# Kernel tuning notes

Measured on AMD Instinct MI355X. Metric: run time of the kernel, lower is better.

Reference implementation:

```python
import jax, jax.numpy as jnp
import numpy as np

Q, L = 512, 4096


def setup_inputs() -> dict:
    key = jax.random.key(0)
    ks = jax.random.split(key, 12)
    def rn(k, shape, s=0.05):
        return jax.random.normal(k, shape, jnp.float32) * s
    return {
        "reactions": jax.random.normal(ks[0], (1, Q, 256), jnp.float32),
        "protein":   jax.random.normal(ks[1], (1, L, 1024), jnp.float32),
        # conv1d(1024->256, k=1) == pointwise linear
        "Wc":  rn(ks[2], (256, 1024)), "bc":  jnp.zeros((256,), jnp.float32),
        "W1":  rn(ks[3], (64, 256)),   "b1":  jnp.zeros((64,), jnp.float32),
        "W2":  rn(ks[4], (64, 256)),   "b2":  jnp.zeros((64,), jnp.float32),
        "Wa":  rn(ks[5], (64, 64)),    "ba":  jnp.zeros((64,), jnp.float32),
        "Wpa": rn(ks[6], (64, 64)),    "bpa": jnp.zeros((64,), jnp.float32),
        "Wra": rn(ks[7], (64, 64)),    "bra": jnp.zeros((64,), jnp.float32),
        "Wf1": rn(ks[8], (256, 128)),  "bf1": jnp.zeros((256,), jnp.float32),
        "Wf2": rn(ks[9], (128, 256)),  "bf2": jnp.zeros((128,), jnp.float32),
        "Wf3": rn(ks[10], (1, 128)),   "bf3": jnp.zeros((1,), jnp.float32),
    }


def reference(reactions, protein, Wc, bc, W1, b1, W2, b2, Wa, ba,
              Wpa, bpa, Wra, bra, Wf1, bf1, Wf2, bf2, Wf3, bf3):
    # protein: [1, L, 1024] -> 1x1 conv over channels == linear -> [L, 256]
    p = jax.nn.relu(protein[0] @ Wc.T + bc)
    # reactions: [1, Q, 256] -> [Q, 64]
    r = jax.nn.relu(reactions[0] @ W2.T + b2)
    # protein tokens -> [L, 64]
    k = jax.nn.relu(p @ W1.T + b1)

    ra = r @ Wra.T + bra            # [Q, 64]
    pa = k @ Wpa.T + bpa            # [L, 64]
    # broadcast outer-sum + relu + small linear: [Q, L, 64]
    A = jax.nn.relu(ra[:, None, :] + pa[None, :, :]) @ Wa.T + ba

    r_gate = jax.nn.sigmoid(jnp.mean(A, axis=1))   # [Q, 64]
    p_gate = jax.nn.sigmoid(jnp.mean(A, axis=0))   # [L, 64]

    rxnfp = r + r * r_gate                          # [Q, 64]
    prot = jnp.max(k + k * p_gate, axis=0)          # [64]  maxpool over L

    ctx = jnp.concatenate(
        [rxnfp, jnp.broadcast_to(prot, (rxnfp.shape[0], 64))], axis=1)  # [Q,128]

    # dropout layers are identity in eval mode
    h = jax.nn.leaky_relu(ctx @ Wf1.T + bf1)
    h = jax.nn.leaky_relu(h @ Wf2.T + bf2)
    out = h @ Wf3.T + bf3
    return out.reshape(-1)                          # [Q]
```

## Files before the change

### kernel.cpp

```cpp
#include <hip/hip_runtime.h>
#include <hip/hip_bf16.h>
#include <math.h>

#define TPB 256

typedef __attribute__((ext_vector_type(8))) short s16x8;
typedef __attribute__((ext_vector_type(4))) float f32x4;

#define MFMA16(a, b, c) __builtin_amdgcn_mfma_f32_16x16x32_bf16((a), (b), (c), 0, 0, 0)

constexpr unsigned OFF_P    = 0u;
constexpr unsigned OFF_K    = OFF_P    + 4096u*256u;
constexpr unsigned OFF_PA   = OFF_K    + 4096u*64u;
constexpr unsigned OFF_R    = OFF_PA   + 4096u*64u;
constexpr unsigned OFF_RA   = OFF_R    + 512u*64u;
constexpr unsigned OFF_SR   = OFF_RA   + 512u*64u;
constexpr unsigned OFF_PMAX = OFF_SR   + 512u*64u;

__device__ __forceinline__ short f2bf(float x) {
  union { float f; unsigned u; } v; v.f = x;
  unsigned r = v.u + 0x7FFFu + ((v.u >> 16) & 1u);
  return (short)(r >> 16);
}
__device__ __forceinline__ unsigned pkbf(float a, float b) {
  __hip_bfloat162 h = __float22bfloat162_rn(make_float2(a, b));
  union { __hip_bfloat162 h2; unsigned u; } v; v.h2 = h;
  return v.u;
}
union U8 { s16x8 s; unsigned u[4]; };

__global__ __launch_bounds__(TPB, 2) void k1_gemm(
    const float* __restrict__ prot, const float* __restrict__ Wc,
    const float* __restrict__ bc,   float* __restrict__ ws)
{
  int bid = blockIdx.x;
  int tid = threadIdx.x;
  if (bid >= 512) {
    int tb = bid - 512;
    unsigned base = OFF_SR + (unsigned)tb * 16384u;
#pragma unroll
    for (int it = 0; it < 16; ++it) {
      int idx = it * TPB + tid;
      *(float4*)&ws[base + (unsigned)idx * 4u] = make_float4(0.f, 0.f, 0.f, 0.f);
    }
    if (tb == 1 && tid < 16)
      *(float4*)&ws[OFF_PMAX + tid * 4] = make_float4(0.f, 0.f, 0.f, 0.f);
    return;
  }

  __shared__ __align__(16) short Asm[32 * 72];
  __shared__ __align__(16) short Bsm[64 * 72];

  int m0 = (bid >> 2) * 32;
  int n0 = (bid & 3) * 64;
  int wave = tid >> 6, lane = tid & 63;
  int wm = (wave & 1) * 16, wn = (wave >> 1) * 32;
  int lm = lane & 15, quad = lane >> 4;

  int arow = tid >> 3, aseg = (tid & 7) * 8;
  int brow = tid >> 2, bseg = (tid & 3) * 16;

  const float* Ag = prot + (size_t)(m0 + arow) * 1024 + aseg;
  const float* Bg = Wc   + (size_t)(n0 + brow) * 1024 + bseg;

  float4 a4[2], b4[4];
#pragma unroll
  for (int i = 0; i < 2; ++i) a4[i] = *(const float4*)(Ag + i * 4);
#pragma unroll
  for (int i = 0; i < 4; ++i) b4[i] = *(const float4*)(Bg + i * 4);

  f32x4 acc[2] = {};

  for (int kc = 0; kc < 16; ++kc) {
    __syncthreads();
    {
      U8 s;
      s.u[0] = pkbf(a4[0].x, a4[0].y); s.u[1] = pkbf(a4[0].z, a4[0].w);
      s.u[2] = pkbf(a4[1].x, a4[1].y); s.u[3] = pkbf(a4[1].z, a4[1].w);
      *(s16x8*)&Asm[arow * 72 + aseg] = s.s;
    }
#pragma unroll
    for (int h = 0; h < 2; ++h) {
      U8 s;
      s.u[0] = pkbf(b4[h*2].x,   b4[h*2].y);
      s.u[1] = pkbf(b4[h*2].z,   b4[h*2].w);
      s.u[2] = pkbf(b4[h*2+1].x, b4[h*2+1].y);
      s.u[3] = pkbf(b4[h*2+1].z, b4[h*2+1].w);
      *(s16x8*)&Bsm[brow * 72 + bseg + h * 8] = s.s;
    }
    if (kc < 15) {
#pragma unroll
      for (int i = 0; i < 2; ++i) a4[i] = *(const float4*)(Ag + (kc + 1) * 64 + i * 4);
#pragma unroll
      for (int i = 0; i < 4; ++i) b4[i] = *(const float4*)(Bg + (kc + 1) * 64 + i * 4);
    }
    __syncthreads();
#pragma unroll
    for (int ks = 0; ks < 2; ++ks) {
      s16x8 af = *(const s16x8*)&Asm[(wm + lm) * 72 + ks * 32 + quad * 8];
#pragma unroll
      for (int ni = 0; ni < 2; ++ni) {
        s16x8 bfv = *(const s16x8*)&Bsm[(wn + ni * 16 + lm) * 72 + ks * 32 + quad * 8];
        acc[ni] = MFMA16(af, bfv, acc[ni]);
      }
    }
  }

#pragma unroll
  for (int ni = 0; ni < 2; ++ni) {
    int col = n0 + wn + ni * 16 + lm;
    float bcv = bc[col];
#pragma unroll
    for (int r = 0; r < 4; ++r) {
      int row = m0 + wm + quad * 4 + r;
      ws[OFF_P + (unsigned)row * 256u + col] = fmaxf(acc[ni][r] + bcv, 0.f);
    }
  }
}

__global__ __launch_bounds__(TPB, 2) void k2_heads(
    const float* __restrict__ reactions,
    const float* __restrict__ W1,  const float* __restrict__ b1,
    const float* __restrict__ W2,  const float* __restrict__ b2,
    const float* __restrict__ Wpa, const float* __restrict__ bpa,
    const float* __restrict__ Wra, const float* __restrict__ bra,
    float* __restrict__ ws)
{
  __shared__ __align__(16) short Asm[32 * 264];
  __shared__ __align__(16) short Bsm[64 * 264];
  __shared__ __align__(16) short Ksm[32 * 72];
  __shared__ __align__(16) short Wsm[64 * 72];
  int bid = blockIdx.x, tid = threadIdx.x;
  bool isProt = bid < 128;
  int row0 = (isProt ? bid : (bid - 128)) * 32;
  const float* src  = isProt ? (ws + OFF_P) : reactions;
  const float* Wst1 = isProt ? W1 : W2;
  const float* bv   = isProt ? b1 : b2;
  const float* Wst2 = isProt ? Wpa : Wra;
  const float* b2nd = isProt ? bpa : bra;
  float* out1 = ws + (isProt ? OFF_K : OFF_R);
  float* out2 = ws + (isProt ? OFF_PA : OFF_RA);

  {
    int row = tid >> 3, seg = (tid & 7) * 32;
    const float* sp = src + (size_t)(row0 + row) * 256 + seg;
    float4 f[8];
#pragma unroll
    for (int i = 0; i < 8; ++i) f[i] = *(const float4*)(sp + i * 4);
#pragma unroll
    for (int i = 0; i < 4; ++i) {
      U8 s;
      s.u[0] = pkbf(f[2*i].x,   f[2*i].y);
      s.u[1] = pkbf(f[2*i].z,   f[2*i].w);
      s.u[2] = pkbf(f[2*i+1].x, f[2*i+1].y);
      s.u[3] = pkbf(f[2*i+1].z, f[2*i+1].w);
      *(s16x8*)&Asm[row * 264 + seg + i * 8] = s.s;
    }
  }
  {
    int row = tid >> 2, seg = (tid & 3) * 64;
    const float* sp = Wst1 + (size_t)row * 256 + seg;
#pragma unroll
    for (int i = 0; i < 8; ++i) {
      float4 fa = *(const float4*)(sp + i * 8);
      float4 fb = *(const float4*)(sp + i * 8 + 4);
      U8 s;
      s.u[0] = pkbf(fa.x, fa.y); s.u[1] = pkbf(fa.z, fa.w);
      s.u[2] = pkbf(fb.x, fb.y); s.u[3] = pkbf(fb.z, fb.w);
      *(s16x8*)&Bsm[row * 264 + seg + i * 8] = s.s;
    }
  }
  {
    int row = tid >> 2, seg = (tid & 3) * 16;
    const float* sp = Wst2 + (size_t)row * 64 + seg;
#pragma unroll
    for (int i = 0; i < 2; ++i) {
      float4 fa = *(const float4*)(sp + i * 8);
      float4 fb = *(const float4*)(sp + i * 8 + 4);
      U8 s;
      s.u[0] = pkbf(fa.x, fa.y); s.u[1] = pkbf(fa.z, fa.w);
      s.u[2] = pkbf(fb.x, fb.y); s.u[3] = pkbf(fb.z, fb.w);
      *(s16x8*)&Wsm[row * 72 + seg + i * 8] = s.s;
    }
  }
  __syncthreads();

  int wave = tid >> 6, lane = tid & 63;
  int lm = lane & 15, quad = lane >> 4;
  int wm = (wave >> 1) * 16, wn = (wave & 1) * 32;

  f32x4 acc[2] = {};
#pragma unroll
  for (int kc = 0; kc < 8; ++kc) {
    s16x8 a = *(const s16x8*)&Asm[(wm + lm) * 264 + kc * 32 + quad * 8];
#pragma unroll
    for (int ni = 0; ni < 2; ++ni) {
      s16x8 b = *(const s16x8*)&Bsm[(wn + ni * 16 + lm) * 264 + kc * 32 + quad * 8];
      acc[ni] = MFMA16(a, b, acc[ni]);
    }
  }
#pragma unroll
  for (int ni = 0; ni < 2; ++ni) {
    int col = wn + ni * 16 + lm;
    float bb = bv[col];
#pragma unroll
    for (int r = 0; r < 4; ++r) {
      int row = wm + quad * 4 + r;
      float kv = fmaxf(acc[ni][r] + bb, 0.f);
      out1[(size_t)(row0 + row) * 64 + col] = kv;
      Ksm[row * 72 + col] = f2bf(kv);
    }
  }
  __syncthreads();

  f32x4 acc2[2] = {};
#pragma unroll
  for (int kc = 0; kc < 2; ++kc) {
    s16x8 a = *(const s16x8*)&Ksm[(wm + lm) * 72 + kc * 32 + quad * 8];
#pragma unroll
    for (int ni = 0; ni < 2; ++ni) {
      s16x8 b = *(const s16x8*)&Wsm[(wn + ni * 16 + lm) * 72 + kc * 32 + quad * 8];
      acc2[ni] = MFMA16(a, b, acc2[ni]);
    }
  }
#pragma unroll
  for (int ni = 0; ni < 2; ++ni) {
    int col = wn + ni * 16 + lm;
    float bb = b2nd[col];
#pragma unroll
    for (int r = 0; r < 4; ++r) {
      int row = wm + quad * 4 + r;
      out2[(size_t)(row0 + row) * 64 + col] = acc2[ni][r] + bb;
    }
  }
}

__global__ __launch_bounds__(TPB) void k3_interact(
    const float* __restrict__ Wa, const float* __restrict__ ba,
    float* __restrict__ ws)
{
  __shared__ float sm[9280];
  int bid = blockIdx.x, tid = threadIdx.x;
  int c = tid & 63, g = tid >> 6;
  const float* ra = ws + OFF_RA;
  const float* pa = ws + OFF_PA;

  if (bid < 256) {
    int qt = bid >> 3, ls = bid & 7;
    int q0 = qt * 16, l0 = ls * 512;
    float u[4], acc[4];
#pragma unroll
    for (int i = 0; i < 4; ++i) {
      u[i] = ra[(q0 + g * 4 + i) * 64u + c];
      acc[i] = 0.f;
    }
    for (int chunk = 0; chunk < 8; ++chunk) {
      unsigned base = (unsigned)(l0 + chunk * 64) * 64u;
      for (int it = 0; it < 4; ++it) {
        int i4 = it * TPB + tid;
        int row = i4 >> 4, c4 = (i4 & 15) * 4;
        *(float4*)&sm[row * 64 + c4] = *(const float4*)(pa + base + row * 64 + c4);
      }
      __syncthreads();
#pragma unroll 4
      for (int ll = 0; ll < 64; ++ll) {
        float x = sm[ll * 64 + c];
#pragma unroll
        for (int i = 0; i < 4; ++i) acc[i] += fmaxf(u[i] + x, 0.f);
      }
      __syncthreads();
    }
#pragma unroll
    for (int i = 0; i < 4; ++i)
      atomicAdd(&ws[OFF_SR + (unsigned)(q0 + g * 4 + i) * 64u + c], acc[i]);
  } else {
    int b = bid - 256;
    int l0 = b * 16;
    for (int it = 0; it < 16; ++it) {
      int idx = it * TPB + tid;
      int a = idx >> 6, bb = idx & 63;
      sm[5120 + bb * 65 + a] = Wa[idx];
    }
    float v[4], acc[4];
#pragma unroll
    for (int i = 0; i < 4; ++i) {
      v[i] = pa[(unsigned)(l0 + g * 4 + i) * 64u + c];
      acc[i] = 0.f;
    }
    for (int chunk = 0; chunk < 8; ++chunk) {
      unsigned base = (unsigned)(chunk * 64) * 64u;
      for (int it = 0; it < 4; ++it) {
        int i4 = it * TPB + tid;
        int row = i4 >> 4, c4 = (i4 & 15) * 4;
        *(float4*)&sm[row * 64 + c4] = *(const float4*)(ra + base + row * 64 + c4);
      }
      __syncthreads();
#pragma unroll 4
      for (int qq = 0; qq < 64; ++qq) {
        float x = sm[qq * 64 + c];
#pragma unroll
        for (int i = 0; i < 4; ++i) acc[i] += fmaxf(v[i] + x, 0.f);
      }
      __syncthreads();
    }
#pragma unroll
    for (int i = 0; i < 4; ++i) sm[4096 + (g * 4 + i) * 64 + c] = acc[i];
    __syncthreads();
    float vmax = 0.f;
    float bac = ba[c];
#pragma unroll
    for (int i = 0; i < 4; ++i) {
      int ll = g * 4 + i;
      float dot = 0.f;
#pragma unroll 8
      for (int jj = 0; jj < 64; ++jj)
        dot += sm[4096 + ll * 64 + jj] * sm[5120 + jj * 65 + c];
      float pg = 1.f / (1.f + __expf(-(dot * (1.f / 512.f) + bac)));
      float val = ws[OFF_K + (unsigned)(l0 + ll) * 64u + c] * (1.f + pg);
      vmax = fmaxf(vmax, val);
    }
    atomicMax((int*)&ws[OFF_PMAX + c], __float_as_int(vmax));
  }
}

__global__ __launch_bounds__(TPB) void k4_final(
    const float* __restrict__ Wa,  const float* __restrict__ ba,
    const float* __restrict__ Wf1, const float* __restrict__ bf1,
    const float* __restrict__ Wf2, const float* __restrict__ bf2,
    const float* __restrict__ Wf3, const float* __restrict__ bf3,
    float* __restrict__ ws, float* __restrict__ out)
{
  __shared__ __align__(16) short mrb[16 * 72];
  __shared__ __align__(16) short wab[64 * 72];
  __shared__ __align__(16) short ctxb[16 * 136];
  __shared__ __align__(16) short h1b[16 * 264];
  __shared__ __align__(16) short wgt[256 * 136];
  __shared__ float red[64];
  int bid = blockIdx.x, tid = threadIdx.x;
  int q0 = bid * 16;
  int wave = tid >> 6, lane = tid & 63;
  int lm = lane & 15, quad = lane >> 4;

  {
    int q = tid >> 4, c4 = (tid & 15) * 4;
    float4 v = *(const float4*)&ws[OFF_SR + (unsigned)(q0 + q) * 64u + c4];
    uint2 st = make_uint2(pkbf(v.x * (1.f/4096.f), v.y * (1.f/4096.f)),
                          pkbf(v.z * (1.f/4096.f), v.w * (1.f/4096.f)));
    *(uint2*)&mrb[q * 72 + c4] = st;
  }
#pragma unroll
  for (int it = 0; it < 4; ++it) {
    int i4 = it * TPB + tid;
    int row = i4 >> 4, c4 = (i4 & 15) * 4;
    float4 v = *(const float4*)&Wa[row * 64 + c4];
    uint2 st = make_uint2(pkbf(v.x, v.y), pkbf(v.z, v.w));
    *(uint2*)&wab[row * 72 + c4] = st;
  }
  __syncthreads();

  f32x4 gacc = {};
#pragma unroll
  for (int kc = 0; kc < 2; ++kc) {
    s16x8 a = *(const s16x8*)&mrb[lm * 72 + kc * 32 + quad * 8];
    s16x8 b = *(const s16x8*)&wab[(wave * 16 + lm) * 72 + kc * 32 + quad * 8];
    gacc = MFMA16(a, b, gacc);
  }
  {
    int c = wave * 16 + lm;
    float bac = ba[c];
    short pb = f2bf(ws[OFF_PMAX + c]);
#pragma unroll
    for (int r = 0; r < 4; ++r) {
      int q = quad * 4 + r;
      float gg = 1.f / (1.f + __expf(-(gacc[r] + bac)));
      float rv = ws[OFF_R + (unsigned)(q0 + q) * 64u + c];
      ctxb[q * 136 + c]      = f2bf(rv * (1.f + gg));
      ctxb[q * 136 + 64 + c] = pb;
    }
  }
#pragma unroll 4
  for (int it = 0; it < 32; ++it) {
    int i4 = it * TPB + tid;
    int row = i4 >> 5, c4 = (i4 & 31) * 4;
    float4 v = *(const float4*)&Wf1[row * 128 + c4];
    uint2 st = make_uint2(pkbf(v.x, v.y), pkbf(v.z, v.w));
    *(uint2*)&wgt[row * 136 + c4] = st;
  }
  __syncthreads();

  f32x4 h[4] = {};
#pragma unroll
  for (int kc = 0; kc < 4; ++kc) {
    s16x8 a = *(const s16x8*)&ctxb[lm * 136 + kc * 32 + quad * 8];
#pragma unroll
    for (int nt = 0; nt < 4; ++nt) {
      s16x8 b = *(const s16x8*)&wgt[(wave * 64 + nt * 16 + lm) * 136 + kc * 32 + quad * 8];
      h[nt] = MFMA16(a, b, h[nt]);
    }
  }
#pragma unroll
  for (int nt = 0; nt < 4; ++nt) {
    int n = wave * 64 + nt * 16 + lm;
    float bb = bf1[n];
#pragma unroll
    for (int r = 0; r < 4; ++r) {
      int q = quad * 4 + r;
      float v = h[nt][r] + bb;
      v = v > 0.f ? v : 0.01f * v;
      h1b[q * 264 + n] = f2bf(v);
    }
  }
  __syncthreads();

#pragma unroll 4
  for (int it = 0; it < 32; ++it) {
    int i4 = it * TPB + tid;
    int row = i4 >> 6, c4 = (i4 & 63) * 4;
    float4 v = *(const float4*)&Wf2[row * 256 + c4];
    uint2 st = make_uint2(pkbf(v.x, v.y), pkbf(v.z, v.w));
    *(uint2*)&wgt[row * 264 + c4] = st;
  }
  __syncthreads();

  f32x4 o[2] = {};
#pragma unroll
  for (int kc = 0; kc < 8; ++kc) {
    s16x8 a = *(const s16x8*)&h1b[lm * 264 + kc * 32 + quad * 8];
#pragma unroll
    for (int nt = 0; nt < 2; ++nt) {
      s16x8 b = *(const s16x8*)&wgt[(wave * 32 + nt * 16 + lm) * 264 + kc * 32 + quad * 8];
      o[nt] = MFMA16(a, b, o[nt]);
    }
  }
  float pv[4] = {0.f, 0.f, 0.f, 0.f};
#pragma unroll
  for (int nt = 0; nt < 2; ++nt) {
    int m = wave * 32 + nt * 16 + lm;
    float bb = bf2[m], w3 = Wf3[m];
#pragma unroll
    for (int r = 0; r < 4; ++r) {
      float v = o[nt][r] + bb;
      v = v > 0.f ? v : 0.01f * v;
      pv[r] += v * w3;
    }
  }
#pragma unroll
  for (int msk = 1; msk < 16; msk <<= 1)
#pragma unroll
    for (int r = 0; r < 4; ++r) pv[r] += __shfl_xor(pv[r], msk);
  if (lm == 0) {
#pragma unroll
    for (int r = 0; r < 4; ++r) red[(quad * 4 + r) * 4 + wave] = pv[r];
  }
  __syncthreads();
  if (tid < 16)
    out[q0 + tid] = red[tid * 4] + red[tid * 4 + 1] + red[tid * 4 + 2] +
                    red[tid * 4 + 3] + bf3[0];
}

extern "C" void kernel_launch(void* const* d_in, const int* in_sizes, int n_in,
                              void* d_out, int out_size, void* d_ws, size_t ws_size,
                              hipStream_t stream)
{
  const float* reactions = (const float*)d_in[0];
  const float* protein   = (const float*)d_in[1];
  const float* Wc  = (const float*)d_in[2];
  const float* bc  = (const float*)d_in[3];
  const float* W1  = (const float*)d_in[4];
  const float* b1  = (const float*)d_in[5];
  const float* W2  = (const float*)d_in[6];
  const float* b2  = (const float*)d_in[7];
  const float* Wa  = (const float*)d_in[8];
  const float* ba  = (const float*)d_in[9];
  const float* Wpa = (const float*)d_in[10];
  const float* bpa = (const float*)d_in[11];
  const float* Wra = (const float*)d_in[12];
  const float* bra = (const float*)d_in[13];
  const float* Wf1 = (const float*)d_in[14];
  const float* bf1 = (const float*)d_in[15];
  const float* Wf2 = (const float*)d_in[16];
  const float* bf2 = (const float*)d_in[17];
  const float* Wf3 = (const float*)d_in[18];
  const float* bf3 = (const float*)d_in[19];
  float* ws  = (float*)d_ws;
  float* out = (float*)d_out;

  hipLaunchKernelGGL(k1_gemm, dim3(514), dim3(TPB), 0, stream,
                     protein, Wc, bc, ws);
  hipLaunchKernelGGL(k2_heads, dim3(144), dim3(TPB), 0, stream,
                     reactions, W1, b1, W2, b2, Wpa, bpa, Wra, bra, ws);
  hipLaunchKernelGGL(k3_interact, dim3(512), dim3(TPB), 0, stream,
                     Wa, ba, ws);
  hipLaunchKernelGGL(k4_final, dim3(32), dim3(TPB), 0, stream,
                     Wa, ba, Wf1, bf1, Wf2, bf2, Wf3, bf3, ws, out);
}
```

Measured before the change: 178.8 us.

## Double-buffer shared tiles with register prefetch and split interaction work finer

The interaction kernel now prefetches the next 64-row tile into registers while computing on the current shared-memory buffer, using two ping-pong buffers so only one barrier is needed per chunk. The row-sum blocks are split into twice as many blocks, each covering 256 L positions, and the grid grows to 768 blocks. Launch bounds request higher occupancy. The aim is to hide global-load latency and fill more CUs, at the cost of extra registers and twice as many atomic adds into the row sums.

```diff
diff --git a/kernel.cpp b/kernel.cpp
--- a/kernel.cpp
+++ b/kernel.cpp
@@ -235,76 +235,114 @@
   }
 }
 
-__global__ __launch_bounds__(TPB) void k3_interact(
+__global__ __launch_bounds__(TPB, 4) void k3_interact(
     const float* __restrict__ Wa, const float* __restrict__ ba,
     float* __restrict__ ws)
 {
-  __shared__ float sm[9280];
+  __shared__ float sm[8192];
   int bid = blockIdx.x, tid = threadIdx.x;
   int c = tid & 63, g = tid >> 6;
   const float* ra = ws + OFF_RA;
   const float* pa = ws + OFF_PA;
 
-  if (bid < 256) {
-    int qt = bid >> 3, ls = bid & 7;
-    int q0 = qt * 16, l0 = ls * 512;
+  int srow = tid >> 4, sc4 = (tid & 15) * 4;
+
+  if (bid < 512) {
+    int qt = bid >> 4, ls = bid & 15;
+    int q0 = qt * 16, l0 = ls * 256;
+    const float* src = pa + (size_t)l0 * 64;
     float u[4], acc[4];
 #pragma unroll
     for (int i = 0; i < 4; ++i) {
       u[i] = ra[(q0 + g * 4 + i) * 64u + c];
       acc[i] = 0.f;
     }
-    for (int chunk = 0; chunk < 8; ++chunk) {
-      unsigned base = (unsigned)(l0 + chunk * 64) * 64u;
-      for (int it = 0; it < 4; ++it) {
-        int i4 = it * TPB + tid;
-        int row = i4 >> 4, c4 = (i4 & 15) * 4;
-        *(float4*)&sm[row * 64 + c4] = *(const float4*)(pa + base + row * 64 + c4);
-      }
-      __syncthreads();
+    float4 a4[4];
+#pragma unroll
+    for (int it = 0; it < 4; ++it)
+      a4[it] = *(const float4*)(src + (it * 16 + srow) * 64 + sc4);
+#pragma unroll
+    for (int it = 0; it < 4; ++it)
+      *(float4*)&sm[(it * 16 + srow) * 64 + sc4] = a4[it];
+#pragma unroll
+    for (int it = 0; it < 4; ++it)
+      a4[it] = *(const float4*)(src + 4096 + (it * 16 + srow) * 64 + sc4);
+    __syncthreads();
+
+    for (int ck = 0; ck < 4; ++ck) {
+      const float* buf = sm + (ck & 1) * 4096;
 #pragma unroll 4
       for (int ll = 0; ll < 64; ++ll) {
-        float x = sm[ll * 64 + c];
+        float x = buf[ll * 64 + c];
 #pragma unroll
         for (int i = 0; i < 4; ++i) acc[i] += fmaxf(u[i] + x, 0.f);
       }
-      __syncthreads();
+      if (ck < 3) {
+        float* nbuf = sm + ((ck + 1) & 1) * 4096;
+#pragma unroll
+        for (int it = 0; it < 4; ++it)
+          *(float4*)&nbuf[(it * 16 + srow) * 64 + sc4] = a4[it];
+        if (ck < 2) {
+#pragma unroll
+          for (int it = 0; it < 4; ++it)
+            a4[it] = *(const float4*)(src + (ck + 2) * 4096 + (it * 16 + srow) * 64 + sc4);
+        }
+        __syncthreads();
+      }
     }
 #pragma unroll
     for (int i = 0; i < 4; ++i)
       atomicAdd(&ws[OFF_SR + (unsigned)(q0 + g * 4 + i) * 64u + c], acc[i]);
   } else {
-    int b = bid - 256;
+    int b = bid - 512;
     int l0 = b * 16;
+    float v[4], acc[4];
+#pragma unroll
+    for (int i = 0; i < 4; ++i) {
+      v[i] = pa[(unsigned)(l0 + g * 4 + i) * 64u + c];
+      acc[i] = 0.f;
+    }
+    float4 a4[4];
+#pragma unroll
+    for (int it = 0; it < 4; ++it)
+      a4[it] = *(const float4*)(ra + (it * 16 + srow) * 64 + sc4);
+#pragma unroll
+    for (int it = 0; it < 4; ++it)
+      *(float4*)&sm[(it * 16 + srow) * 64 + sc4] = a4[it];
+#pragma unroll
+    for (int it = 0; it < 4; ++it)
+      a4[it] = *(const float4*)(ra + 4096 + (it * 16 + srow) * 64 + sc4);
+    __syncthreads();
+
+    for (int ck = 0; ck < 8; ++ck) {
+      const float* buf = sm + (ck & 1) * 4096;
+#pragma unroll 4
+      for (int qq = 0; qq < 64; ++qq) {
+        float x = buf[qq * 64 + c];
+#pragma unroll
+        for (int i = 0; i < 4; ++i) acc[i] += fmaxf(v[i] + x, 0.f);
+      }
+      if (ck < 7) {
+        float* nbuf = sm + ((ck + 1) & 1) * 4096;
+#pragma unroll
+        for (int it = 0; it < 4; ++it)
+          *(float4*)&nbuf[(it * 16 + srow) * 64 + sc4] = a4[it];
+        if (ck < 6) {
+#pragma unroll
+          for (int it = 0; it < 4; ++it)
+            a4[it] = *(const float4*)(ra + (ck + 2) * 4096 + (it * 16 + srow) * 64 + sc4);
+        }
+        __syncthreads();
+      }
+    }
+    __syncthreads();
+#pragma unroll
+    for (int i = 0; i < 4; ++i) sm[(g * 4 + i) * 64 + c] = acc[i];
     for (int it = 0; it < 16; ++it) {
       int idx = it * TPB + tid;
       int a = idx >> 6, bb = idx & 63;
-      sm[5120 + bb * 65 + a] = Wa[idx];
-    }
-    float v[4], acc[4];
-#pragma unroll
-    for (int i = 0; i < 4; ++i) {
-      v[i] = pa[(unsigned)(l0 + g * 4 + i) * 64u + c];
-      acc[i] = 0.f;
-    }
-    for (int chunk = 0; chunk < 8; ++chunk) {
-      unsigned base = (unsigned)(chunk * 64) * 64u;
-      for (int it = 0; it < 4; ++it) {
-        int i4 = it * TPB + tid;
-        int row = i4 >> 4, c4 = (i4 & 15) * 4;
-        *(float4*)&sm[row * 64 + c4] = *(const float4*)(ra + base + row * 64 + c4);
-      }
-      __syncthreads();
-#pragma unroll 4
-      for (int qq = 0; qq < 64; ++qq) {
-        float x = sm[qq * 64 + c];
-#pragma unroll
-        for (int i = 0; i < 4; ++i) acc[i] += fmaxf(v[i] + x, 0.f);
-      }
-      __syncthreads();
-    }
-#pragma unroll
-    for (int i = 0; i < 4; ++i) sm[4096 + (g * 4 + i) * 64 + c] = acc[i];
+      sm[1024 + bb * 65 + a] = Wa[idx];
+    }
     __syncthreads();
     float vmax = 0.f;
     float bac = ba[c];
@@ -314,7 +352,7 @@
       float dot = 0.f;
 #pragma unroll 8
       for (int jj = 0; jj < 64; ++jj)
-        dot += sm[4096 + ll * 64 + jj] * sm[5120 + jj * 65 + c];
+        dot += sm[ll * 64 + jj] * sm[1024 + jj * 65 + c];
       float pg = 1.f / (1.f + __expf(-(dot * (1.f / 512.f) + bac)));
       float val = ws[OFF_K + (unsigned)(l0 + ll) * 64u + c] * (1.f + pg);
       vmax = fmaxf(vmax, val);
@@ -489,7 +527,7 @@
                      protein, Wc, bc, ws);
   hipLaunchKernelGGL(k2_heads, dim3(144), dim3(TPB), 0, stream,
                      reactions, W1, b1, W2, b2, Wpa, bpa, Wra, bra, ws);
-  hipLaunchKernelGGL(k3_interact, dim3(512), dim3(TPB), 0, stream,
+  hipLaunchKernelGGL(k3_interact, dim3(768), dim3(TPB), 0, stream,
                      Wa, ba, ws);
   hipLaunchKernelGGL(k4_final, dim3(32), dim3(TPB), 0, stream,
                      Wa, ba, Wf1, bf1, Wf2, bf2, Wf3, bf3, ws, out);
```

Result: slower. 183.1 us (+2.4%).

## Rebalance interaction kernel work split and drop chunked LDS staging

Applied to the files above, without the earlier changes.

Restructures k3_interact: the per-L branch now streams ra straight from global memory (cached) with no shared-memory staging or barriers, and is placed first. The per-Q sum branch is split into 1024 smaller blocks, each loading one 128-row pa tile once, giving a 1280-block grid. Launch bounds now request 4 blocks per CU and shared memory is reduced to raise occupancy. The cost is more atomicAdd traffic on the Q sums and uncoalesced strided global reads of ra in the L branch.

```diff
diff --git a/kernel.cpp b/kernel.cpp
--- a/kernel.cpp
+++ b/kernel.cpp
@@ -235,76 +235,38 @@
   }
 }
 
-__global__ __launch_bounds__(TPB) void k3_interact(
+__global__ __launch_bounds__(TPB, 4) void k3_interact(
     const float* __restrict__ Wa, const float* __restrict__ ba,
     float* __restrict__ ws)
 {
-  __shared__ float sm[9280];
+  __shared__ float sm[8192];
   int bid = blockIdx.x, tid = threadIdx.x;
   int c = tid & 63, g = tid >> 6;
   const float* ra = ws + OFF_RA;
   const float* pa = ws + OFF_PA;
 
   if (bid < 256) {
-    int qt = bid >> 3, ls = bid & 7;
-    int q0 = qt * 16, l0 = ls * 512;
-    float u[4], acc[4];
+    int l0 = bid * 16;
+    float v[4], acc[4];
 #pragma unroll
     for (int i = 0; i < 4; ++i) {
-      u[i] = ra[(q0 + g * 4 + i) * 64u + c];
+      v[i] = pa[(unsigned)(l0 + g * 4 + i) * 64u + c];
       acc[i] = 0.f;
     }
-    for (int chunk = 0; chunk < 8; ++chunk) {
-      unsigned base = (unsigned)(l0 + chunk * 64) * 64u;
-      for (int it = 0; it < 4; ++it) {
-        int i4 = it * TPB + tid;
-        int row = i4 >> 4, c4 = (i4 & 15) * 4;
-        *(float4*)&sm[row * 64 + c4] = *(const float4*)(pa + base + row * 64 + c4);
-      }
-      __syncthreads();
-#pragma unroll 4
-      for (int ll = 0; ll < 64; ++ll) {
-        float x = sm[ll * 64 + c];
-#pragma unroll
-        for (int i = 0; i < 4; ++i) acc[i] += fmaxf(u[i] + x, 0.f);
-      }
-      __syncthreads();
-    }
-#pragma unroll
-    for (int i = 0; i < 4; ++i)
-      atomicAdd(&ws[OFF_SR + (unsigned)(q0 + g * 4 + i) * 64u + c], acc[i]);
-  } else {
-    int b = bid - 256;
-    int l0 = b * 16;
+    const float* rap = ra + c;
+#pragma unroll 8
+    for (int q = 0; q < 512; ++q) {
+      float x = rap[q * 64];
+#pragma unroll
+      for (int i = 0; i < 4; ++i) acc[i] += fmaxf(v[i] + x, 0.f);
+    }
+#pragma unroll
+    for (int i = 0; i < 4; ++i) sm[(g * 4 + i) * 64 + c] = acc[i];
     for (int it = 0; it < 16; ++it) {
       int idx = it * TPB + tid;
       int a = idx >> 6, bb = idx & 63;
-      sm[5120 + bb * 65 + a] = Wa[idx];
-    }
-    float v[4], acc[4];
-#pragma unroll
-    for (int i = 0; i < 4; ++i) {
-      v[i] = pa[(unsigned)(l0 + g * 4 + i) * 64u + c];
-      acc[i] = 0.f;
-    }
-    for (int chunk = 0; chunk < 8; ++chunk) {
-      unsigned base = (unsigned)(chunk * 64) * 64u;
-      for (int it = 0; it < 4; ++it) {
-        int i4 = it * TPB + tid;
-        int row = i4 >> 4, c4 = (i4 & 15) * 4;
-        *(float4*)&sm[row * 64 + c4] = *(const float4*)(ra + base + row * 64 + c4);
-      }
-      __syncthreads();
-#pragma unroll 4
-      for (int qq = 0; qq < 64; ++qq) {
-        float x = sm[qq * 64 + c];
-#pragma unroll
-        for (int i = 0; i < 4; ++i) acc[i] += fmaxf(v[i] + x, 0.f);
-      }
-      __syncthreads();
-    }
-#pragma unroll
-    for (int i = 0; i < 4; ++i) sm[4096 + (g * 4 + i) * 64 + c] = acc[i];
+      sm[1024 + bb * 65 + a] = Wa[idx];
+    }
     __syncthreads();
     float vmax = 0.f;
     float bac = ba[c];
@@ -314,12 +276,39 @@
       float dot = 0.f;
 #pragma unroll 8
       for (int jj = 0; jj < 64; ++jj)
-        dot += sm[4096 + ll * 64 + jj] * sm[5120 + jj * 65 + c];
+        dot += sm[ll * 64 + jj] * sm[1024 + jj * 65 + c];
       float pg = 1.f / (1.f + __expf(-(dot * (1.f / 512.f) + bac)));
       float val = ws[OFF_K + (unsigned)(l0 + ll) * 64u + c] * (1.f + pg);
       vmax = fmaxf(vmax, val);
     }
     atomicMax((int*)&ws[OFF_PMAX + c], __float_as_int(vmax));
+  } else {
+    int b = bid - 256;
+    int qt = b >> 5, ls = b & 31;
+    int q0 = qt * 16, l0 = ls * 128;
+    int srow = tid >> 4, sc4 = (tid & 15) * 4;
+    const float* src = pa + (size_t)l0 * 64;
+#pragma unroll
+    for (int it = 0; it < 8; ++it) {
+      int row = it * 16 + srow;
+      *(float4*)&sm[row * 64 + sc4] = *(const float4*)(src + row * 64 + sc4);
+    }
+    float u[4], acc[4];
+#pragma unroll
+    for (int i = 0; i < 4; ++i) {
+      u[i] = ra[(unsigned)(q0 + g * 4 + i) * 64u + c];
+      acc[i] = 0.f;
+    }
+    __syncthreads();
+#pragma unroll 8
+    for (int l = 0; l < 128; ++l) {
+      float x = sm[l * 64 + c];
+#pragma unroll
+      for (int i = 0; i < 4; ++i) acc[i] += fmaxf(u[i] + x, 0.f);
+    }
+#pragma unroll
+    for (int i = 0; i < 4; ++i)
+      atomicAdd(&ws[OFF_SR + (unsigned)(q0 + g * 4 + i) * 64u + c], acc[i]);
   }
 }
 
@@ -489,7 +478,7 @@
                      protein, Wc, bc, ws);
   hipLaunchKernelGGL(k2_heads, dim3(144), dim3(TPB), 0, stream,
                      reactions, W1, b1, W2, b2, Wpa, bpa, Wra, bra, ws);
-  hipLaunchKernelGGL(k3_interact, dim3(512), dim3(TPB), 0, stream,
+  hipLaunchKernelGGL(k3_interact, dim3(1280), dim3(TPB), 0, stream,
                      Wa, ba, ws);
   hipLaunchKernelGGL(k4_final, dim3(32), dim3(TPB), 0, stream,
                      Wa, ba, Wf1, bf1, Wf2, bf2, Wf3, bf3, ws, out);
```

After: 172.9 us. -3.3%, faster.
